# Kernel tuning notes

Hardware: AMD Instinct MI355X
Metric: run time of the kernel (lower is better)

The kernel has to match this reference:

```python
import jax, jax.numpy as jnp
import numpy as np

A, B, OBS, ACT, H, G = 8, 4096, 512, 64, 1024, 64
N, E = 10000, 40000
NODE, GH, NTYPES, AEMB = 32, 64, 8, 16


def _ln(x, g, b, eps=1e-5):
    m = jnp.mean(x, -1, keepdims=True)
    v = jnp.mean((x - m) ** 2, -1, keepdims=True)
    return (x - m) * jax.lax.rsqrt(v + eps) * g + b


def _neigh_mean(h, edges, n):
    # undirected mean aggregation: each dependency edge contributes both ways
    s, d = edges[:, 0], edges[:, 1]
    agg = jnp.zeros((n, h.shape[-1]), h.dtype).at[d].add(h[s]).at[s].add(h[d])
    deg = jnp.zeros((n,), h.dtype).at[d].add(1.0).at[s].add(1.0)
    return agg / jnp.maximum(deg, 1.0)[:, None]


def setup_inputs() -> dict:
    key = jax.random.key(0)
    ks = jax.random.split(key, 32)
    f32 = jnp.float32

    def w(k, i, o):
        return (jax.random.normal(k, (i, o), f32) / np.sqrt(i)).astype(f32)

    d = {}
    d["observations"] = jax.random.normal(ks[0], (A, B, OBS), f32)
    d["node_types"] = jax.random.randint(ks[1], (N,), 0, NTYPES)
    d["node_agents"] = jax.random.randint(ks[2], (N,), 0, A)
    d["edges"] = jax.random.randint(ks[3], (E, 2), 0, N)
    # graph encoder params
    d["type_embed"] = (jax.random.normal(ks[4], (NTYPES, NODE), f32) * 0.02).astype(f32)
    d["gagent_embed"] = (jax.random.normal(ks[5], (A, NODE), f32) * 0.02).astype(f32)
    d["W_l0"] = w(ks[6], 2 * NODE, GH); d["b_l0"] = jnp.zeros((GH,), f32)
    d["g_l0"] = jnp.ones((GH,), f32);   d["be_l0"] = jnp.zeros((GH,), f32)
    d["W_l1"] = w(ks[7], GH + GH, G);   d["b_l1"] = jnp.zeros((G,), f32)
    d["g_l1"] = jnp.ones((G,), f32);    d["be_l1"] = jnp.zeros((G,), f32)
    d["W_gp"] = w(ks[8], G, G);         d["b_gp"] = jnp.zeros((G,), f32)
    # shared policy params
    d["agent_embed"] = (jax.random.normal(ks[9], (A, AEMB), f32) * 0.02).astype(f32)
    d["Wp1"] = w(ks[10], OBS + G + AEMB, H); d["bp1"] = jnp.zeros((H,), f32)
    d["Wp2"] = w(ks[11], H, H);              d["bp2"] = jnp.zeros((H,), f32)
    d["Wp3"] = w(ks[12], H, ACT);            d["bp3"] = jnp.zeros((ACT,), f32)
    # value head params
    d["Wv1"] = w(ks[13], OBS * A + G, H); d["bv1"] = jnp.zeros((H,), f32)
    d["Wv2"] = w(ks[14], H, H);           d["bv2"] = jnp.zeros((H,), f32)
    d["Wv3"] = w(ks[15], H, 1);           d["bv3"] = jnp.zeros((1,), f32)
    return d


def _forward(observations, node_types, node_agents, edges,
             type_embed, gagent_embed, W_l0, b_l0, g_l0, be_l0,
             W_l1, b_l1, g_l1, be_l1, W_gp, b_gp,
             agent_embed, Wp1, bp1, Wp2, bp2, Wp3, bp3,
             Wv1, bv1, Wv2, bv2, Wv3, bv3):
    # --- graph encoder ---
    x = jnp.concatenate([type_embed[node_types], gagent_embed[node_agents]], -1)  # [N,64]
    # layer 0: aggregation is computed-but-ignored in the original; combined = x
    h = _ln(jax.nn.relu(x @ W_l0 + b_l0), g_l0, be_l0)                 # [N,GH]
    agg = _neigh_mean(h, edges, N)                                     # [N,GH]
    h = _ln(jax.nn.relu(jnp.concatenate([h, agg], -1) @ W_l1 + b_l1), g_l1, be_l1)  # [N,G]
    graph_embed = jnp.mean(h, 0) @ W_gp + b_gp                         # [G]

    ge = jnp.broadcast_to(graph_embed, (B, G))                         # [B,G]
    # --- shared policy over agents ---
    ae = jnp.broadcast_to(agent_embed[:, None, :], (A, B, AEMB))
    geA = jnp.broadcast_to(graph_embed, (A, B, G))
    comb = jnp.concatenate([observations, geA, ae], -1)                # [A,B,OBS+G+16]
    hp = jax.nn.relu(jnp.einsum("abi,io->abo", comb, Wp1) + bp1)
    hp = jax.nn.relu(jnp.einsum("abi,io->abo", hp, Wp2) + bp2)
    logits = jnp.einsum("abi,io->abo", hp, Wp3) + bp3                  # [A,B,ACT]
    # --- value head ---
    joint = jnp.transpose(observations, (1, 0, 2)).reshape(B, A * OBS)
    vin = jnp.concatenate([joint, ge], -1)                             # [B, A*OBS+G]
    hv = jax.nn.relu(vin @ Wv1 + bv1)
    hv = jax.nn.relu(hv @ Wv2 + bv2)
    value = hv @ Wv3 + bv3                                             # [B,1]
    return logits, value


def reference(observations, node_types, node_agents, edges,
              type_embed, gagent_embed, W_l0, b_l0, g_l0, be_l0,
              W_l1, b_l1, g_l1, be_l1, W_gp, b_gp,
              agent_embed, Wp1, bp1, Wp2, bp2, Wp3, bp3,
              Wv1, bv1, Wv2, bv2, Wv3, bv3):
    return _forward(observations, node_types, node_agents, edges,
                    type_embed, gagent_embed, W_l0, b_l0, g_l0, be_l0,
                    W_l1, b_l1, g_l1, be_l1, W_gp, b_gp,
                    agent_embed, Wp1, bp1, Wp2, bp2, Wp3, bp3,
                    Wv1, bv1, Wv2, bv2, Wv3, bv3)
```

## Files before the change

### kernel.cpp

```cpp
#include <hip/hip_runtime.h>
#include <hip/hip_bf16.h>

#define A_ 8
#define B_ 4096
#define OBS_ 512
#define ACT_ 64
#define H_ 1024
#define G_ 64
#define N_ 10000
#define E_ 40000

using bf16 = __hip_bfloat16;
typedef __attribute__((ext_vector_type(8))) short short8;
typedef __attribute__((ext_vector_type(4))) float f32x4;

__device__ __forceinline__ float wsum(float v) {
#pragma unroll
  for (int off = 32; off >= 1; off >>= 1) v += __shfl_xor(v, off, 64);
  return v;
}

__device__ __forceinline__ void storeC(float* p, float v) { *p = v; }
__device__ __forceinline__ void storeC(bf16* p, float v) { *p = __float2bfloat16(v); }

__device__ __forceinline__ unsigned short f2bu(float x) {
  bf16 h = __float2bfloat16(x);
  unsigned short u;
  __builtin_memcpy(&u, &h, 2);
  return u;
}

__device__ __forceinline__ void gload_lds16(const bf16* g, const void* lds_uniform) {
  __builtin_amdgcn_global_load_lds(
      (const __attribute__((address_space(1))) unsigned int*)g,
      (__attribute__((address_space(3))) unsigned int*)lds_uniform, 16, 0, 0);
}

template <int N>
__device__ __forceinline__ void waitvm() {
#define WV_CASE(n) if constexpr (N == n) asm volatile("s_waitcnt vmcnt(" #n ")" ::: "memory");
  WV_CASE(0) WV_CASE(3) WV_CASE(4) WV_CASE(6) WV_CASE(8) WV_CASE(9) WV_CASE(12) WV_CASE(16)
  static_assert(N == 0 || N == 3 || N == 4 || N == 6 || N == 8 || N == 9 || N == 12 || N == 16,
                "vmcnt value not in table");
#undef WV_CASE
}

__global__ void gnn_l0_k(const int* __restrict__ node_types, const int* __restrict__ node_agents,
                         const float* __restrict__ type_embed, const float* __restrict__ gagent_embed,
                         const float* __restrict__ W, const float* __restrict__ b,
                         const float* __restrict__ g, const float* __restrict__ be,
                         float* __restrict__ h0, float* __restrict__ agg, float* __restrict__ deg) {
  int n = blockIdx.x, t = threadIdx.x;
  __shared__ float x[64];
  int ty = node_types[n], ag = node_agents[n];
  x[t] = (t < 32) ? type_embed[ty * 32 + t] : gagent_embed[ag * 32 + (t - 32)];
  agg[(size_t)n * 64 + t] = 0.f;
  if (t == 0) deg[n] = 0.f;
  __syncthreads();
  float acc = b[t];
#pragma unroll 8
  for (int i = 0; i < 64; i++) acc += x[i] * W[i * 64 + t];
  acc = fmaxf(acc, 0.f);
  float m = wsum(acc) * (1.f / 64.f);
  float d = acc - m;
  float v = wsum(d * d) * (1.f / 64.f);
  h0[(size_t)n * 64 + t] = d * rsqrtf(v + 1e-5f) * g[t] + be[t];
}

__global__ void edge_k(const int* __restrict__ edges, const float* __restrict__ h0,
                       float* __restrict__ agg, float* __restrict__ deg) {
  int idx = blockIdx.x * 256 + threadIdx.x;
  if (idx >= E_ * 64) return;
  int e = idx >> 6, c = idx & 63;
  int s = edges[e * 2 + 0], d = edges[e * 2 + 1];
  atomicAdd(&agg[(size_t)d * 64 + c], h0[(size_t)s * 64 + c]);
  atomicAdd(&agg[(size_t)s * 64 + c], h0[(size_t)d * 64 + c]);
  if (c == 0) { atomicAdd(&deg[d], 1.f); atomicAdd(&deg[s], 1.f); }
}

__global__ void gnn_l1_k(const float* __restrict__ h0, const float* __restrict__ agg,
                         const float* __restrict__ deg, const float* __restrict__ W,
                         const float* __restrict__ b, const float* __restrict__ g,
                         const float* __restrict__ be, float* __restrict__ h1) {
  int n = blockIdx.x, t = threadIdx.x;
  __shared__ float x[128];
  x[t] = h0[(size_t)n * 64 + t];
  x[64 + t] = agg[(size_t)n * 64 + t] / fmaxf(deg[n], 1.0f);
  __syncthreads();
  float acc = b[t];
#pragma unroll 8
  for (int i = 0; i < 128; i++) acc += x[i] * W[i * 64 + t];
  acc = fmaxf(acc, 0.f);
  float m = wsum(acc) * (1.f / 64.f);
  float d = acc - m;
  float v = wsum(d * d) * (1.f / 64.f);
  h1[(size_t)n * 64 + t] = d * rsqrtf(v + 1e-5f) * g[t] + be[t];
}

__global__ void colmean_k(const float* __restrict__ h1, float* __restrict__ meanv) {
  int c = blockIdx.x, t = threadIdx.x;
  float s = 0.f;
  for (int n = t; n < N_; n += 256) s += h1[(size_t)n * 64 + c];
  __shared__ float red[256];
  red[t] = s;
  __syncthreads();
  for (int off = 128; off >= 1; off >>= 1) {
    if (t < off) red[t] += red[t + off];
    __syncthreads();
  }
  if (t == 0) meanv[c] = red[0] / (float)N_;
}

__global__ void fused_bias_k(const float* __restrict__ meanv, const float* __restrict__ Wgp,
                             const float* __restrict__ bgp, const float* __restrict__ agent_embed,
                             const float* __restrict__ Wp1, const float* __restrict__ bp1,
                             const float* __restrict__ Wv1, const float* __restrict__ bv1,
                             float* __restrict__ biasA, float* __restrict__ biasV) {
  __shared__ float ge[64];
  int t = threadIdx.x;
  if (t < 64) {
    float s = bgp[t];
    for (int g2 = 0; g2 < 64; g2++) s += meanv[g2] * Wgp[g2 * 64 + t];
    ge[t] = s;
  }
  __syncthreads();
  int blk = blockIdx.x;
  if (blk < 32) {
    int idx = blk * 256 + t;
    int a = idx >> 10, o = idx & 1023;
    float s = bp1[o];
    for (int g2 = 0; g2 < 64; g2++) s += ge[g2] * Wp1[(size_t)(512 + g2) * 1024 + o];
    for (int e = 0; e < 16; e++) s += agent_embed[a * 16 + e] * Wp1[(size_t)(576 + e) * 1024 + o];
    biasA[idx] = s;
  } else {
    int o = (blk - 32) * 256 + t;
    float s = bv1[o];
    for (int g2 = 0; g2 < 64; g2++) s += ge[g2] * Wv1[(size_t)(4096 + g2) * 1024 + o];
    biasV[o] = s;
  }
}

__global__ void conv_joint_k(const float* __restrict__ obs, bf16* __restrict__ joint) {
  size_t i = ((size_t)blockIdx.x * 256 + threadIdx.x) * 8;
  int a = (int)(i >> 21);
  int rem = (int)(i & ((1u << 21) - 1));
  int b = rem >> 9, k = rem & 511;
  const float* p = obs + i;
  short8 o;
#pragma unroll
  for (int t = 0; t < 8; t++) o[t] = (short)f2bu(p[t]);
  *(short8*)(joint + (size_t)b * 4096 + a * 512 + k) = o;
}

__global__ void wtrans_k(const float* __restrict__ W, bf16* __restrict__ Wt, int K, int N) {
  __shared__ float t[32][33];
  int n0 = blockIdx.x * 32, k0 = blockIdx.y * 32;
  int tx = threadIdx.x & 31, ty = threadIdx.x >> 5;
#pragma unroll
  for (int r = ty; r < 32; r += 8) t[r][tx] = W[(size_t)(k0 + r) * N + n0 + tx];
  __syncthreads();
#pragma unroll
  for (int r = ty; r < 32; r += 8) Wt[(size_t)(n0 + r) * K + k0 + tx] = __float2bfloat16(t[tx][r]);
}

template <int FM, int FN, int WAVES_M, int WAVES_N, int DEPTH, int AMODE, int BIASMODE, bool RELU,
          typename TC>
__launch_bounds__(WAVES_M * WAVES_N * 64, 2)
__global__ void pgemm_k(const bf16* __restrict__ Ap, const bf16* __restrict__ Bt,
                        const float* __restrict__ biasp, TC* __restrict__ Cp,
                        int M, int N, int K) {
  constexpr int NTHR = WAVES_M * WAVES_N * 64;
  constexpr int AR = WAVES_M * FM * 16;
  constexpr int BR = WAVES_N * FN * 16;
  constexpr int RPG = NTHR / 4;
  constexpr int AG = AR / RPG;
  constexpr int BG = BR / RPG;
  constexpr int G = AG + BG;
  constexpr int GRP = NTHR * 16;
  constexpr int ABYTES = AR * 64;
  constexpr int SBUF = (AR + BR) * 64;
  constexpr int NB = DEPTH + 1;
  __shared__ char smem[NB * SBUF];

  const int tid = threadIdx.x;
  const int wid = tid >> 6, lane = tid & 63;
  const int wm = wid / WAVES_N, wn = wid % WAVES_N;
  const int l15 = lane & 15;

  const int nwg = gridDim.x * gridDim.y;
  int fid = blockIdx.y * gridDim.x + blockIdx.x;
  int swz = (fid & 7) * (nwg >> 3) + (fid >> 3);
  const int m0 = (swz / gridDim.x) * AR;
  const int n0 = (swz % gridDim.x) * BR;

  f32x4 acc[FM][FN];
#pragma unroll
  for (int i = 0; i < FM; i++)
#pragma unroll
    for (int j = 0; j < FN; j++) acc[i][j] = (f32x4){0.f, 0.f, 0.f, 0.f};

  const bf16* pa[AG];
  const bf16* pb[BG];
  {
    int row = tid >> 2;
    int c = (tid & 3) ^ ((tid >> 3) & 3);
#pragma unroll
    for (int q = 0; q < AG; ++q) {
      int r = m0 + q * RPG + row;
      if (AMODE == 0)
        pa[q] = Ap + (size_t)r * K + c * 8;
      else
        pa[q] = Ap + (((size_t)(r & (B_ - 1))) << 12) + ((size_t)(r >> 12) << 9) + c * 8;
    }
#pragma unroll
    for (int q = 0; q < BG; ++q) {
      int r = n0 + q * RPG + row;
      pb[q] = Bt + (size_t)r * K + c * 8;
    }
  }

  const int cA = (lane >> 4) ^ ((l15 >> 1) & 3);
  const int offA0 = (wm * FM * 16 + l15) * 64 + cA * 16;
  const int offB0 = ABYTES + (wn * FN * 16 + l15) * 64 + cA * 16;

  auto stage = [&](int buf) {
    char* base = smem + buf * SBUF;
#pragma unroll
    for (int q = 0; q < AG; ++q) {
      gload_lds16(pa[q], base + q * GRP + wid * 1024);
      pa[q] += 32;
    }
#pragma unroll
    for (int q = 0; q < BG; ++q) {
      gload_lds16(pb[q], base + ABYTES + q * GRP + wid * 1024);
      pb[q] += 32;
    }
  };

  auto comp = [&](int buf) {
    const char* sb = smem + buf * SBUF;
    short8 bfr[FN];
#pragma unroll
    for (int j = 0; j < FN; ++j) bfr[j] = *(const short8*)(sb + offB0 + j * 1024);
    constexpr int FH = (FM > 4) ? FM / 2 : FM;
#pragma unroll
    for (int h = 0; h < FM / FH; ++h) {
      short8 afr[FH];
#pragma unroll
      for (int i = 0; i < FH; ++i) afr[i] = *(const short8*)(sb + offA0 + (h * FH + i) * 1024);
      __builtin_amdgcn_s_setprio(1);
#pragma unroll
      for (int i = 0; i < FH; ++i)
#pragma unroll
        for (int j = 0; j < FN; ++j)
          acc[h * FH + i][j] =
              __builtin_amdgcn_mfma_f32_16x16x32_bf16(afr[i], bfr[j], acc[h * FH + i][j], 0, 0, 0);
      __builtin_amdgcn_s_setprio(0);
    }
  };

  const int nt = K >> 5;
#pragma unroll
  for (int q = 0; q < DEPTH; ++q) stage(q);
  int cbuf = 0, sbi = DEPTH;
  for (int T = 0; T < nt - DEPTH; ++T) {
    stage(sbi);
    if (++sbi == NB) sbi = 0;
    waitvm<DEPTH * G>();
    __builtin_amdgcn_s_barrier();
    asm volatile("" ::: "memory");
    comp(cbuf);
    if (++cbuf == NB) cbuf = 0;
    asm volatile("" ::: "memory");
    __builtin_amdgcn_s_barrier();
  }
#define DRAIN(d)                       \
  {                                    \
    waitvm<(d) * G>();                 \
    __builtin_amdgcn_s_barrier();      \
    asm volatile("" ::: "memory");     \
    comp(cbuf);                        \
    if (++cbuf == NB) cbuf = 0;        \
    asm volatile("" ::: "memory");     \
  }
  if constexpr (DEPTH == 4) { DRAIN(3) DRAIN(2) }
  DRAIN(1)
  DRAIN(0)
#undef DRAIN

#pragma unroll
  for (int i = 0; i < FM; ++i) {
    int rb = m0 + wm * FM * 16 + i * 16 + (lane >> 4) * 4;
#pragma unroll
    for (int j = 0; j < FN; ++j) {
      int col = n0 + wn * FN * 16 + j * 16 + l15;
#pragma unroll
      for (int r = 0; r < 4; r++) {
        int row = rb + r;
        float bias = (BIASMODE == 0) ? biasp[col] : biasp[((row >> 12) << 10) + col];
        float v = acc[i][j][r] + bias;
        if (RELU) v = fmaxf(v, 0.f);
        storeC(&Cp[(size_t)row * N + col], v);
      }
    }
  }
}

__global__ void v3_k(const bf16* __restrict__ hv2, const float* __restrict__ Wv3,
                     const float* __restrict__ bv3, float* __restrict__ out) {
  int wid = threadIdx.x >> 6, lane = threadIdx.x & 63;
  int row = blockIdx.x * 4 + wid;
  float s = 0.f;
#pragma unroll
  for (int k = lane; k < 1024; k += 64) s += __bfloat162float(hv2[(size_t)row * 1024 + k]) * Wv3[k];
  s = wsum(s);
  if (lane == 0) out[row] = s + bv3[0];
}

extern "C" void kernel_launch(void* const* d_in, const int* in_sizes, int n_in,
                              void* d_out, int out_size, void* d_ws, size_t ws_size,
                              hipStream_t stream) {
  const float* obs = (const float*)d_in[0];
  const int* node_types = (const int*)d_in[1];
  const int* node_agents = (const int*)d_in[2];
  const int* edges = (const int*)d_in[3];
  const float* type_embed = (const float*)d_in[4];
  const float* gagent_embed = (const float*)d_in[5];
  const float* W_l0 = (const float*)d_in[6];
  const float* b_l0 = (const float*)d_in[7];
  const float* g_l0 = (const float*)d_in[8];
  const float* be_l0 = (const float*)d_in[9];
  const float* W_l1 = (const float*)d_in[10];
  const float* b_l1 = (const float*)d_in[11];
  const float* g_l1 = (const float*)d_in[12];
  const float* be_l1 = (const float*)d_in[13];
  const float* W_gp = (const float*)d_in[14];
  const float* b_gp = (const float*)d_in[15];
  const float* agent_embed = (const float*)d_in[16];
  const float* Wp1 = (const float*)d_in[17];
  const float* bp1 = (const float*)d_in[18];
  const float* Wp2 = (const float*)d_in[19];
  const float* bp2 = (const float*)d_in[20];
  const float* Wp3 = (const float*)d_in[21];
  const float* bp3 = (const float*)d_in[22];
  const float* Wv1 = (const float*)d_in[23];
  const float* bv1 = (const float*)d_in[24];
  const float* Wv2 = (const float*)d_in[25];
  const float* bv2 = (const float*)d_in[26];
  const float* Wv3 = (const float*)d_in[27];
  const float* bv3 = (const float*)d_in[28];

  char* wsp = (char*)d_ws;
  auto alloc = [&](size_t bytes) {
    char* p = wsp;
    wsp += (bytes + 255) & ~(size_t)255;
    return p;
  };
  float* h0 = (float*)alloc((size_t)N_ * 64 * 4);
  float* agg = (float*)alloc((size_t)N_ * 64 * 4);
  float* deg = (float*)alloc((size_t)N_ * 4);
  float* h1 = (float*)alloc((size_t)N_ * 64 * 4);
  float* meanv = (float*)alloc(64 * 4);
  float* biasA = (float*)alloc(8 * 1024 * 4);
  float* biasV = (float*)alloc(1024 * 4);
  bf16* joint = (bf16*)alloc((size_t)4096 * 4096 * 2);
  bf16* Wp1t = (bf16*)alloc((size_t)1024 * 512 * 2);
  bf16* Wp2t = (bf16*)alloc((size_t)1024 * 1024 * 2);
  bf16* Wp3t = (bf16*)alloc((size_t)64 * 1024 * 2);
  bf16* Wv1t = (bf16*)alloc((size_t)1024 * 4096 * 2);
  bf16* Wv2t = (bf16*)alloc((size_t)1024 * 1024 * 2);
  bf16* C1 = (bf16*)alloc((size_t)32768 * 1024 * 2);
  bf16* C2 = (bf16*)alloc((size_t)32768 * 1024 * 2);
  bf16* hv = (bf16*)alloc((size_t)4096 * 1024 * 2);
  bf16* hv2 = (bf16*)alloc((size_t)4096 * 1024 * 2);

  float* logits = (float*)d_out;
  float* value = (float*)d_out + (size_t)A_ * B_ * ACT_;

  gnn_l0_k<<<N_, 64, 0, stream>>>(node_types, node_agents, type_embed, gagent_embed, W_l0, b_l0,
                                  g_l0, be_l0, h0, agg, deg);
  edge_k<<<(E_ * 64) / 256, 256, 0, stream>>>(edges, h0, agg, deg);
  gnn_l1_k<<<N_, 64, 0, stream>>>(h0, agg, deg, W_l1, b_l1, g_l1, be_l1, h1);
  colmean_k<<<64, 256, 0, stream>>>(h1, meanv);
  fused_bias_k<<<36, 256, 0, stream>>>(meanv, W_gp, b_gp, agent_embed, Wp1, bp1, Wv1, bv1, biasA,
                                       biasV);

  conv_joint_k<<<(A_ * B_ * OBS_) / 8 / 256, 256, 0, stream>>>(obs, joint);
  wtrans_k<<<dim3(1024 / 32, 512 / 32), 256, 0, stream>>>(Wp1, Wp1t, 512, 1024);
  wtrans_k<<<dim3(1024 / 32, 1024 / 32), 256, 0, stream>>>(Wp2, Wp2t, 1024, 1024);
  wtrans_k<<<dim3(64 / 32, 1024 / 32), 256, 0, stream>>>(Wp3, Wp3t, 1024, 64);
  wtrans_k<<<dim3(1024 / 32, 4096 / 32), 256, 0, stream>>>(Wv1, Wv1t, 4096, 1024);
  wtrans_k<<<dim3(1024 / 32, 1024 / 32), 256, 0, stream>>>(Wv2, Wv2t, 1024, 1024);

  pgemm_k<8, 4, 2, 2, 2, 1, 1, true, bf16>
      <<<dim3(8, 128), 256, 0, stream>>>(joint, Wp1t, biasA, C1, 32768, 1024, 512);
  pgemm_k<8, 4, 2, 2, 2, 0, 0, true, bf16>
      <<<dim3(8, 128), 256, 0, stream>>>(C1, Wp2t, bp2, C2, 32768, 1024, 1024);
  pgemm_k<4, 2, 2, 2, 4, 0, 0, false, float>
      <<<dim3(1, 256), 256, 0, stream>>>(C2, Wp3t, bp3, logits, 32768, 64, 1024);
  pgemm_k<4, 4, 2, 2, 4, 0, 0, true, bf16>
      <<<dim3(8, 32), 256, 0, stream>>>(joint, Wv1t, biasV, hv, 4096, 1024, 4096);
  pgemm_k<4, 4, 2, 2, 4, 0, 0, true, bf16>
      <<<dim3(8, 32), 256, 0, stream>>>(hv, Wv2t, bv2, hv2, 4096, 1024, 1024);
  v3_k<<<1024, 256, 0, stream>>>(hv2, Wv3, bv3, value);
}
```

Before: 305.9 us.

## Add 256x256 8-wave triple-buffered GEMM kernel for the large policy layers

Adds a new GEMM kernel with 256x256 output tiles, 8 waves, three LDS stages, interleaved staging loads and MFMA phases separated by barriers, and s_setprio around MFMA bursts. It replaces the two large policy GEMMs and adds an XCD-style workgroup swizzle. The value-head GEMMs are also relaunched with 512 threads and a different wave split. The goal is more operand reuse per tile and better overlap of loads with matrix work. The cost is lower occupancy (one block per CU) and more barrier traffic.

```diff
diff --git a/kernel.cpp b/kernel.cpp
--- a/kernel.cpp
+++ b/kernel.cpp
@@ -39,9 +39,9 @@
 template <int N>
 __device__ __forceinline__ void waitvm() {
 #define WV_CASE(n) if constexpr (N == n) asm volatile("s_waitcnt vmcnt(" #n ")" ::: "memory");
-  WV_CASE(0) WV_CASE(3) WV_CASE(4) WV_CASE(6) WV_CASE(8) WV_CASE(9) WV_CASE(12) WV_CASE(16)
-  static_assert(N == 0 || N == 3 || N == 4 || N == 6 || N == 8 || N == 9 || N == 12 || N == 16,
-                "vmcnt value not in table");
+  WV_CASE(0) WV_CASE(1) WV_CASE(2) WV_CASE(3) WV_CASE(4) WV_CASE(5) WV_CASE(6) WV_CASE(7)
+  WV_CASE(8) WV_CASE(9) WV_CASE(10) WV_CASE(12) WV_CASE(16)
+  static_assert(N <= 16, "vmcnt too large");
 #undef WV_CASE
 }
 
@@ -161,6 +161,149 @@
   __syncthreads();
 #pragma unroll
   for (int r = ty; r < 32; r += 8) Wt[(size_t)(n0 + r) * K + k0 + tx] = __float2bfloat16(t[tx][r]);
+}
+
+#define MM1(i, j, af, bf) \
+  acc[i][j] = __builtin_amdgcn_mfma_f32_16x16x32_bf16(af, bf, acc[i][j], 0, 0, 0)
+#define MM4x2(h, v)                                                         \
+  MM1((h) * 4 + 0, (v) * 2 + 0, afr0, bfr0); MM1((h) * 4 + 0, (v) * 2 + 1, afr0, bfr1); \
+  MM1((h) * 4 + 1, (v) * 2 + 0, afr1, bfr0); MM1((h) * 4 + 1, (v) * 2 + 1, afr1, bfr1); \
+  MM1((h) * 4 + 2, (v) * 2 + 0, afr2, bfr0); MM1((h) * 4 + 2, (v) * 2 + 1, afr2, bfr1); \
+  MM1((h) * 4 + 3, (v) * 2 + 0, afr3, bfr0); MM1((h) * 4 + 3, (v) * 2 + 1, afr3, bfr1)
+
+#define BAR()                          \
+  __builtin_amdgcn_s_barrier();        \
+  asm volatile("" ::: "memory")
+
+#define G8_BODY(WN_, STG_)                                                       \
+  {                                                                              \
+    const char* sb = smem + cbuf * SBUF;                                         \
+    char* so = smem + sbi * SBUF;                                                \
+    short8 afr0, afr1, afr2, afr3, bfr0, bfr1;                                   \
+                                                                \
+    if (STG_) { gload_lds16(pA0, so + wid * 1024); pA0 += 32; }                  \
+    waitvm<WN_>();                                                               \
+    BAR();                                                                       \
+    afr0 = *(const short8*)(sb + offA + 0 * 1024);                               \
+    afr1 = *(const short8*)(sb + offA + 1 * 1024);                               \
+    afr2 = *(const short8*)(sb + offA + 2 * 1024);                               \
+    afr3 = *(const short8*)(sb + offA + 3 * 1024);                               \
+    bfr0 = *(const short8*)(sb + offB + 0 * 1024);                               \
+    bfr1 = *(const short8*)(sb + offB + 1 * 1024);                               \
+    BAR();                                                                       \
+    __builtin_amdgcn_s_setprio(1);                                               \
+    MM4x2(0, 0);                                                                 \
+    __builtin_amdgcn_s_setprio(0);                                               \
+    BAR();                                                                       \
+                                                                \
+    if (STG_) { gload_lds16(pA1, so + 8192 + wid * 1024); pA1 += 32; }           \
+    bfr0 = *(const short8*)(sb + offB + 2 * 1024);                               \
+    bfr1 = *(const short8*)(sb + offB + 3 * 1024);                               \
+    BAR();                                                                       \
+    __builtin_amdgcn_s_setprio(1);                                               \
+    MM4x2(0, 1);                                                                 \
+    __builtin_amdgcn_s_setprio(0);                                               \
+    BAR();                                                                       \
+                                                                \
+    if (STG_) { gload_lds16(pB0, so + ABYTES + wid * 1024); pB0 += 32; }         \
+    afr0 = *(const short8*)(sb + offA + 4 * 1024);                               \
+    afr1 = *(const short8*)(sb + offA + 5 * 1024);                               \
+    afr2 = *(const short8*)(sb + offA + 6 * 1024);                               \
+    afr3 = *(const short8*)(sb + offA + 7 * 1024);                               \
+    BAR();                                                                       \
+    __builtin_amdgcn_s_setprio(1);                                               \
+    MM4x2(1, 1);                                                                 \
+    __builtin_amdgcn_s_setprio(0);                                               \
+    BAR();                                                                       \
+                                                                \
+    if (STG_) { gload_lds16(pB1, so + ABYTES + 8192 + wid * 1024); pB1 += 32; }  \
+    bfr0 = *(const short8*)(sb + offB + 0 * 1024);                               \
+    bfr1 = *(const short8*)(sb + offB + 1 * 1024);                               \
+    BAR();                                                                       \
+    __builtin_amdgcn_s_setprio(1);                                               \
+    MM4x2(1, 0);                                                                 \
+    __builtin_amdgcn_s_setprio(0);                                               \
+    BAR();                                                                       \
+    if (++cbuf == 3) cbuf = 0;                                                   \
+    if (STG_) { if (++sbi == 3) sbi = 0; }                                       \
+  }
+
+template <int AMODE, int BIASMODE, bool RELU, typename TC>
+__launch_bounds__(512, 1)
+__global__ void g8_k(const bf16* __restrict__ Ap, const bf16* __restrict__ Bt,
+                     const float* __restrict__ biasp, TC* __restrict__ Cp,
+                     int M, int N, int K) {
+  constexpr int SBUF = 512 * 64;
+  constexpr int ABYTES = 256 * 64;
+  __shared__ char smem[3 * SBUF];
+
+  const int tid = threadIdx.x;
+  const int wid = tid >> 6, lane = tid & 63;
+  const int wm = wid >> 2, wn = wid & 3;
+  const int l15 = lane & 15;
+
+  const int nwg = gridDim.x * gridDim.y;
+  int fid = blockIdx.y * gridDim.x + blockIdx.x;
+  int swz = (fid & 7) * (nwg >> 3) + (fid >> 3);
+  const int m0 = (swz / gridDim.x) * 256;
+  const int n0 = (swz % gridDim.x) * 256;
+
+  f32x4 acc[8][4];
+#pragma unroll
+  for (int i = 0; i < 8; i++)
+#pragma unroll
+    for (int j = 0; j < 4; j++) acc[i][j] = (f32x4){0.f, 0.f, 0.f, 0.f};
+
+  const bf16 *pA0, *pA1, *pB0, *pB1;
+  {
+    int row = tid >> 2;
+    int c = (tid & 3) ^ ((tid >> 3) & 3);
+    int rA0 = m0 + row, rA1 = m0 + 128 + row;
+    if (AMODE == 0) {
+      pA0 = Ap + (size_t)rA0 * K + c * 8;
+      pA1 = Ap + (size_t)rA1 * K + c * 8;
+    } else {
+      pA0 = Ap + (((size_t)(rA0 & (B_ - 1))) << 12) + ((size_t)(rA0 >> 12) << 9) + c * 8;
+      pA1 = Ap + (((size_t)(rA1 & (B_ - 1))) << 12) + ((size_t)(rA1 >> 12) << 9) + c * 8;
+    }
+    pB0 = Bt + (size_t)(n0 + row) * K + c * 8;
+    pB1 = Bt + (size_t)(n0 + 128 + row) * K + c * 8;
+  }
+
+  const int cA = (lane >> 4) ^ ((l15 >> 1) & 3);
+  const int offA = (wm * 128 + l15) * 64 + cA * 16;
+  const int offB = ABYTES + (wn * 64 + l15) * 64 + cA * 16;
+
+  const int nt = K >> 5;
+#pragma unroll
+  for (int b = 0; b < 2; ++b) {
+    char* so = smem + b * SBUF;
+    gload_lds16(pA0, so + wid * 1024); pA0 += 32;
+    gload_lds16(pA1, so + 8192 + wid * 1024); pA1 += 32;
+    gload_lds16(pB0, so + ABYTES + wid * 1024); pB0 += 32;
+    gload_lds16(pB1, so + ABYTES + 8192 + wid * 1024); pB1 += 32;
+  }
+  int cbuf = 0, sbi = 2;
+  for (int T = 0; T < nt - 2; ++T) G8_BODY(5, 1)
+  G8_BODY(4, 0)
+  G8_BODY(0, 0)
+
+#pragma unroll
+  for (int i = 0; i < 8; ++i) {
+    int rb = m0 + wm * 128 + i * 16 + (lane >> 4) * 4;
+#pragma unroll
+    for (int j = 0; j < 4; ++j) {
+      int col = n0 + wn * 64 + j * 16 + l15;
+#pragma unroll
+      for (int r = 0; r < 4; r++) {
+        int row = rb + r;
+        float bias = (BIASMODE == 0) ? biasp[col] : biasp[((row >> 12) << 10) + col];
+        float v = acc[i][j][r] + bias;
+        if (RELU) v = fmaxf(v, 0.f);
+        storeC(&Cp[(size_t)row * N + col], v);
+      }
+    }
+  }
 }
 
 template <int FM, int FN, int WAVES_M, int WAVES_N, int DEPTH, int AMODE, int BIASMODE, bool RELU,
@@ -392,15 +535,15 @@
   wtrans_k<<<dim3(1024 / 32, 4096 / 32), 256, 0, stream>>>(Wv1, Wv1t, 4096, 1024);
   wtrans_k<<<dim3(1024 / 32, 1024 / 32), 256, 0, stream>>>(Wv2, Wv2t, 1024, 1024);
 
-  pgemm_k<8, 4, 2, 2, 2, 1, 1, true, bf16>
-      <<<dim3(8, 128), 256, 0, stream>>>(joint, Wp1t, biasA, C1, 32768, 1024, 512);
-  pgemm_k<8, 4, 2, 2, 2, 0, 0, true, bf16>
-      <<<dim3(8, 128), 256, 0, stream>>>(C1, Wp2t, bp2, C2, 32768, 1024, 1024);
+  g8_k<1, 1, true, bf16>
+      <<<dim3(4, 128), 512, 0, stream>>>(joint, Wp1t, biasA, C1, 32768, 1024, 512);
+  g8_k<0, 0, true, bf16>
+      <<<dim3(4, 128), 512, 0, stream>>>(C1, Wp2t, bp2, C2, 32768, 1024, 1024);
   pgemm_k<4, 2, 2, 2, 4, 0, 0, false, float>
       <<<dim3(1, 256), 256, 0, stream>>>(C2, Wp3t, bp3, logits, 32768, 64, 1024);
-  pgemm_k<4, 4, 2, 2, 4, 0, 0, true, bf16>
-      <<<dim3(8, 32), 256, 0, stream>>>(joint, Wv1t, biasV, hv, 4096, 1024, 4096);
-  pgemm_k<4, 4, 2, 2, 4, 0, 0, true, bf16>
-      <<<dim3(8, 32), 256, 0, stream>>>(hv, Wv2t, bv2, hv2, 4096, 1024, 1024);
+  pgemm_k<4, 2, 2, 4, 4, 0, 0, true, bf16>
+      <<<dim3(8, 32), 512, 0, stream>>>(joint, Wv1t, biasV, hv, 4096, 1024, 4096);
+  pgemm_k<4, 2, 2, 4, 4, 0, 0, true, bf16>
+      <<<dim3(8, 32), 512, 0, stream>>>(hv, Wv2t, bv2, hv2, 4096, 1024, 1024);
   v3_k<<<1024, 256, 0, stream>>>(hv2, Wv3, bv3, value);
 }
```

Measured after the change: 305.9 us. Within noise of the previous version (-0.0%).

## Add 256x256-tile 8-wave GEMM kernel for policy layers, retune value GEMMs

Applied to the files above, without the earlier changes.

Introduces a new GEMM kernel with 256x256 output tiles, 8 waves, a 128KB double-buffered LDS using direct global-to-LDS loads, and MFMA bursts interleaved with staged loads under raised wave priority. A grid swizzle groups workgroups for L2 reuse. It replaces the two large policy-MLP GEMMs. The value-head GEMMs are switched to a 2x4-wave, 512-thread configuration of the existing kernel. The large tile cuts LDS and global traffic per FLOP but allows only one workgroup per CU, and the 512-wide grid underfills the CUs less evenly.

```diff
diff --git a/kernel.cpp b/kernel.cpp
--- a/kernel.cpp
+++ b/kernel.cpp
@@ -39,9 +39,9 @@
 template <int N>
 __device__ __forceinline__ void waitvm() {
 #define WV_CASE(n) if constexpr (N == n) asm volatile("s_waitcnt vmcnt(" #n ")" ::: "memory");
-  WV_CASE(0) WV_CASE(3) WV_CASE(4) WV_CASE(6) WV_CASE(8) WV_CASE(9) WV_CASE(12) WV_CASE(16)
-  static_assert(N == 0 || N == 3 || N == 4 || N == 6 || N == 8 || N == 9 || N == 12 || N == 16,
-                "vmcnt value not in table");
+  WV_CASE(0) WV_CASE(1) WV_CASE(2) WV_CASE(3) WV_CASE(4) WV_CASE(5) WV_CASE(6) WV_CASE(7)
+  WV_CASE(8) WV_CASE(9) WV_CASE(10) WV_CASE(12) WV_CASE(16)
+  static_assert(N <= 16, "vmcnt too large");
 #undef WV_CASE
 }
 
@@ -161,6 +161,150 @@
   __syncthreads();
 #pragma unroll
   for (int r = ty; r < 32; r += 8) Wt[(size_t)(n0 + r) * K + k0 + tx] = __float2bfloat16(t[tx][r]);
+}
+
+#define BARR()                        \
+  asm volatile("" ::: "memory");      \
+  __builtin_amdgcn_s_barrier();       \
+  asm volatile("" ::: "memory")
+
+#define RD8(off) (*(const short8*)(sb + (off)))
+
+#define MMQ(FI0)                                                                     \
+  __builtin_amdgcn_s_setprio(1);                                                     \
+  acc[FI0 + 0][0] = __builtin_amdgcn_mfma_f32_16x16x32_bf16(a0, b0, acc[FI0 + 0][0], 0, 0, 0); \
+  acc[FI0 + 0][1] = __builtin_amdgcn_mfma_f32_16x16x32_bf16(a0, b1, acc[FI0 + 0][1], 0, 0, 0); \
+  acc[FI0 + 0][2] = __builtin_amdgcn_mfma_f32_16x16x32_bf16(a0, b2, acc[FI0 + 0][2], 0, 0, 0); \
+  acc[FI0 + 0][3] = __builtin_amdgcn_mfma_f32_16x16x32_bf16(a0, b3, acc[FI0 + 0][3], 0, 0, 0); \
+  acc[FI0 + 1][0] = __builtin_amdgcn_mfma_f32_16x16x32_bf16(a1, b0, acc[FI0 + 1][0], 0, 0, 0); \
+  acc[FI0 + 1][1] = __builtin_amdgcn_mfma_f32_16x16x32_bf16(a1, b1, acc[FI0 + 1][1], 0, 0, 0); \
+  acc[FI0 + 1][2] = __builtin_amdgcn_mfma_f32_16x16x32_bf16(a1, b2, acc[FI0 + 1][2], 0, 0, 0); \
+  acc[FI0 + 1][3] = __builtin_amdgcn_mfma_f32_16x16x32_bf16(a1, b3, acc[FI0 + 1][3], 0, 0, 0); \
+  acc[FI0 + 2][0] = __builtin_amdgcn_mfma_f32_16x16x32_bf16(a2, b0, acc[FI0 + 2][0], 0, 0, 0); \
+  acc[FI0 + 2][1] = __builtin_amdgcn_mfma_f32_16x16x32_bf16(a2, b1, acc[FI0 + 2][1], 0, 0, 0); \
+  acc[FI0 + 2][2] = __builtin_amdgcn_mfma_f32_16x16x32_bf16(a2, b2, acc[FI0 + 2][2], 0, 0, 0); \
+  acc[FI0 + 2][3] = __builtin_amdgcn_mfma_f32_16x16x32_bf16(a2, b3, acc[FI0 + 2][3], 0, 0, 0); \
+  acc[FI0 + 3][0] = __builtin_amdgcn_mfma_f32_16x16x32_bf16(a3, b0, acc[FI0 + 3][0], 0, 0, 0); \
+  acc[FI0 + 3][1] = __builtin_amdgcn_mfma_f32_16x16x32_bf16(a3, b1, acc[FI0 + 3][1], 0, 0, 0); \
+  acc[FI0 + 3][2] = __builtin_amdgcn_mfma_f32_16x16x32_bf16(a3, b2, acc[FI0 + 3][2], 0, 0, 0); \
+  acc[FI0 + 3][3] = __builtin_amdgcn_mfma_f32_16x16x32_bf16(a3, b3, acc[FI0 + 3][3], 0, 0, 0); \
+  __builtin_amdgcn_s_setprio(0)
+
+template <int AMODE, int BIASMODE, bool RELU, typename TC>
+__launch_bounds__(512, 1)
+__global__ void g10_k(const bf16* __restrict__ Ap, const bf16* __restrict__ Bt,
+                      const float* __restrict__ biasp, TC* __restrict__ Cp,
+                      int M, int N, int K) {
+  constexpr int SBUF = 65536;
+  __shared__ char smem[2 * SBUF];
+
+  const int tid = threadIdx.x;
+  const int wid = tid >> 6, lane = tid & 63;
+  const int wm = wid >> 2, wn = wid & 3;
+  const int l15 = lane & 15;
+
+  const int nwg = gridDim.x * gridDim.y;
+  int fid = blockIdx.y * gridDim.x + blockIdx.x;
+  int swz = (fid & 7) * (nwg >> 3) + (fid >> 3);
+  const int m0 = (swz / gridDim.x) * 256;
+  const int n0 = (swz % gridDim.x) * 256;
+
+  f32x4 acc[8][4];
+#pragma unroll
+  for (int i = 0; i < 8; i++)
+#pragma unroll
+    for (int j = 0; j < 4; j++) acc[i][j] = (f32x4){0.f, 0.f, 0.f, 0.f};
+
+  const bf16* pg[8];
+  {
+    int srow = tid >> 3;
+    int c = (tid & 7) ^ (srow & 7);
+#pragma unroll
+    for (int g = 0; g < 4; ++g) {
+      int r = m0 + g * 64 + srow;
+      if (AMODE == 0)
+        pg[g] = Ap + (size_t)r * K + c * 8;
+      else
+        pg[g] = Ap + (((size_t)(r & (B_ - 1))) << 12) + ((size_t)(r >> 12) << 9) + c * 8;
+    }
+#pragma unroll
+    for (int g = 4; g < 8; ++g) {
+      int r = n0 + (g - 4) * 64 + srow;
+      pg[g] = Bt + (size_t)r * K + c * 8;
+    }
+  }
+
+  const int slot0 = (lane >> 4) ^ (l15 & 7);
+  const int aof0 = (wm * 128 + l15) * 128 + slot0 * 16;
+  const int bof0 = 32768 + (wn * 64 + l15) * 128 + slot0 * 16;
+  const int aof1 = aof0 ^ 64;
+  const int bof1 = bof0 ^ 64;
+
+#define STG(g, buf)                                                    \
+  {                                                                    \
+    gload_lds16(pg[g], smem + (buf) * SBUF + (g) * 8192 + wid * 1024); \
+    pg[g] += 64;                                                       \
+  }
+
+#pragma unroll
+  for (int g = 0; g < 8; ++g) STG(g, 0)
+  waitvm<0>();
+  BARR();
+
+  const int nt = K >> 6;
+  for (int t = 0; t < nt; ++t) {
+    const int cb = t & 1, ob = cb ^ 1;
+    const bool last = (t == nt - 1);
+    const char* sb = smem + cb * SBUF;
+    short8 a0, a1, a2, a3, b0, b1, b2, b3;
+    a0 = RD8(aof0 + 0 * 2048); a1 = RD8(aof0 + 1 * 2048);
+    a2 = RD8(aof0 + 2 * 2048); a3 = RD8(aof0 + 3 * 2048);
+    b0 = RD8(bof0 + 0 * 2048); b1 = RD8(bof0 + 1 * 2048);
+    b2 = RD8(bof0 + 2 * 2048); b3 = RD8(bof0 + 3 * 2048);
+    if (!last) { STG(0, ob) STG(1, ob) }
+    BARR();
+    MMQ(0);
+    BARR();
+    a0 = RD8(aof0 + 4 * 2048); a1 = RD8(aof0 + 5 * 2048);
+    a2 = RD8(aof0 + 6 * 2048); a3 = RD8(aof0 + 7 * 2048);
+    if (!last) { STG(2, ob) STG(3, ob) }
+    BARR();
+    MMQ(4);
+    BARR();
+    a0 = RD8(aof1 + 0 * 2048); a1 = RD8(aof1 + 1 * 2048);
+    a2 = RD8(aof1 + 2 * 2048); a3 = RD8(aof1 + 3 * 2048);
+    b0 = RD8(bof1 + 0 * 2048); b1 = RD8(bof1 + 1 * 2048);
+    b2 = RD8(bof1 + 2 * 2048); b3 = RD8(bof1 + 3 * 2048);
+    if (!last) { STG(4, ob) STG(5, ob) }
+    BARR();
+    MMQ(0);
+    BARR();
+    a0 = RD8(aof1 + 4 * 2048); a1 = RD8(aof1 + 5 * 2048);
+    a2 = RD8(aof1 + 6 * 2048); a3 = RD8(aof1 + 7 * 2048);
+    if (!last) { STG(6, ob) STG(7, ob) }
+    BARR();
+    MMQ(4);
+    if (!last) waitvm<0>();
+    BARR();
+  }
+#undef STG
+
+#pragma unroll
+  for (int i = 0; i < 8; ++i) {
+    int rb = m0 + wm * 128 + i * 16 + (lane >> 4) * 4;
+#pragma unroll
+    for (int j = 0; j < 4; ++j) {
+      int col = n0 + wn * 64 + j * 16 + l15;
+#pragma unroll
+      for (int r = 0; r < 4; r++) {
+        int row = rb + r;
+        float bias = (BIASMODE == 0) ? biasp[col] : biasp[((row >> 12) << 10) + col];
+        float v = acc[i][j][r] + bias;
+        if (RELU) v = fmaxf(v, 0.f);
+        storeC(&Cp[(size_t)row * N + col], v);
+      }
+    }
+  }
 }
 
 template <int FM, int FN, int WAVES_M, int WAVES_N, int DEPTH, int AMODE, int BIASMODE, bool RELU,
@@ -392,15 +536,15 @@
   wtrans_k<<<dim3(1024 / 32, 4096 / 32), 256, 0, stream>>>(Wv1, Wv1t, 4096, 1024);
   wtrans_k<<<dim3(1024 / 32, 1024 / 32), 256, 0, stream>>>(Wv2, Wv2t, 1024, 1024);
 
-  pgemm_k<8, 4, 2, 2, 2, 1, 1, true, bf16>
-      <<<dim3(8, 128), 256, 0, stream>>>(joint, Wp1t, biasA, C1, 32768, 1024, 512);
-  pgemm_k<8, 4, 2, 2, 2, 0, 0, true, bf16>
-      <<<dim3(8, 128), 256, 0, stream>>>(C1, Wp2t, bp2, C2, 32768, 1024, 1024);
+  g10_k<1, 1, true, bf16>
+      <<<dim3(4, 128), 512, 0, stream>>>(joint, Wp1t, biasA, C1, 32768, 1024, 512);
+  g10_k<0, 0, true, bf16>
+      <<<dim3(4, 128), 512, 0, stream>>>(C1, Wp2t, bp2, C2, 32768, 1024, 1024);
   pgemm_k<4, 2, 2, 2, 4, 0, 0, false, float>
       <<<dim3(1, 256), 256, 0, stream>>>(C2, Wp3t, bp3, logits, 32768, 64, 1024);
-  pgemm_k<4, 4, 2, 2, 4, 0, 0, true, bf16>
-      <<<dim3(8, 32), 256, 0, stream>>>(joint, Wv1t, biasV, hv, 4096, 1024, 4096);
-  pgemm_k<4, 4, 2, 2, 4, 0, 0, true, bf16>
-      <<<dim3(8, 32), 256, 0, stream>>>(hv, Wv2t, bv2, hv2, 4096, 1024, 1024);
+  pgemm_k<4, 2, 2, 4, 4, 0, 0, true, bf16>
+      <<<dim3(8, 32), 512, 0, stream>>>(joint, Wv1t, biasV, hv, 4096, 1024, 4096);
+  pgemm_k<4, 2, 2, 4, 4, 0, 0, true, bf16>
+      <<<dim3(8, 32), 512, 0, stream>>>(hv, Wv2t, bv2, hv2, 4096, 1024, 1024);
   v3_k<<<1024, 256, 0, stream>>>(hv2, Wv3, bv3, value);
 }
```

Result: no change. 303.4 us (-0.8%).
